# Optimization experiments

Measured on AMD Instinct MI355X. Metric: run time of the kernel, lower is better.

## Reference

```python
import jax, jax.numpy as jnp
import numpy as np

DIM = 512
INNER = 512          # heads * dim_head = 8 * 64
SCALE = 64 ** -0.5   # dim_head ** -0.5 (module uses this even though attention dim is INNER)
EPS = 1e-5


def _ln(x, g, b):
    m = jnp.mean(x, axis=-1, keepdims=True)
    v = jnp.var(x, axis=-1, keepdims=True)
    return (x - m) * jax.lax.rsqrt(v + EPS) * g + b


def setup_inputs() -> dict:
    key = jax.random.key(0)
    ks = jax.random.split(key, 5)
    B, T, C = 2, 32, 1024
    scaled = lambda k, sh, fan: jax.random.normal(k, sh, jnp.float32) * (fan ** -0.5)
    return {
        "x": jax.random.normal(ks[0], (B, T, C, DIM), jnp.float32),
        "gamma_t": jnp.ones((DIM,), jnp.float32),
        "beta_t": jnp.zeros((DIM,), jnp.float32),
        "w_qkv_t": scaled(ks[1], (DIM, 3 * INNER), DIM),
        "w_out_t": scaled(ks[2], (INNER, DIM), INNER),
        "b_out_t": jnp.zeros((DIM,), jnp.float32),
        "gamma_s": jnp.ones((DIM,), jnp.float32),
        "beta_s": jnp.zeros((DIM,), jnp.float32),
        "w_qkv_s": scaled(ks[3], (DIM, 3 * INNER), DIM),
        "w_out_s": scaled(ks[4], (INNER, DIM), INNER),
        "b_out_s": jnp.zeros((DIM,), jnp.float32),
    }


def reference(x, gamma_t, beta_t, w_qkv_t, w_out_t, b_out_t,
              gamma_s, beta_s, w_qkv_s, w_out_s, b_out_s):
    # ---- temporal attention (attend over t, per spatial token c) ----
    h = _ln(x, gamma_t, beta_t)                              # [b,t,c,D]
    q, k, v = jnp.split(h @ w_qkv_t, 3, axis=-1)             # each [b,t,c,I]
    q, k, v = (jnp.swapaxes(a, 1, 2) for a in (q, k, v))     # [b,c,t,I]
    attn = jax.nn.softmax(jnp.einsum('bcqd,bckd->bcqk', q, k) * SCALE, axis=-1)
    out = jnp.einsum('bcqk,bckd->bcqd', attn, v)             # [b,c,t,I]
    out = out @ w_out_t + b_out_t                            # [b,c,t,D]
    # ---- spatial attention (attend over c, per frame t) ----
    h = _ln(out, gamma_s, beta_s)                            # [b,c,t,D]
    q, k, v = jnp.split(h @ w_qkv_s, 3, axis=-1)             # each [b,c,t,I]
    q, k, v = (jnp.swapaxes(a, 1, 2) for a in (q, k, v))     # [b,t,c,I]
    attn = jax.nn.softmax(jnp.einsum('btqd,btkd->btqk', q, k) * SCALE, axis=-1)
    out = jnp.einsum('btqk,btkd->btqd', attn, v)             # [b,t,c,I]
    return out @ w_out_s + b_out_s                           # [b,t,c,D]
```

## Files before the change

kernel.cpp:

```cpp
#include <hip/hip_runtime.h>
#include <type_traits>

typedef unsigned short u16;
typedef _Float16 f16;
typedef f16 f16x8 __attribute__((ext_vector_type(8)));
typedef unsigned short u16x8 __attribute__((ext_vector_type(8)));
typedef unsigned short u16x4 __attribute__((ext_vector_type(4)));
typedef float f32x4 __attribute__((ext_vector_type(4)));

#define DEV __device__ __forceinline__

DEV u16 f2h(float f) { return __builtin_bit_cast(u16, (f16)f); }
DEV float h2f(u16 u) { return (float)__builtin_bit_cast(f16, u); }

DEV f32x4 mfma_f16(f16x8 a, f16x8 b, f32x4 c) {
  return __builtin_amdgcn_mfma_f32_16x16x32_f16(a, b, c, 0, 0, 0);
}
DEV f16x8 ldf16(const u16* p) { return *(const f16x8*)p; }

DEV void gl2lds16(const u16* g, u16* l) {
  __builtin_amdgcn_global_load_lds((const __attribute__((address_space(1))) void*)g,
                                   (__attribute__((address_space(3))) void*)l, 16, 0, 0);
}

DEV int swz(int row, int col) { return row * 64 + (col ^ ((row & 7) << 3)); }

DEV int xcd_remap(int d, int nwg) { return (d & 7) * (nwg >> 3) + (d >> 3); }

__global__ __launch_bounds__(256)
void wT_all_kernel(const float* __restrict__ Wq_t, const float* __restrict__ Wo_t,
                   const float* __restrict__ Wq_s, const float* __restrict__ Wo_s,
                   u16* __restrict__ Tq_t, u16* __restrict__ To_t,
                   u16* __restrict__ Tq_s, u16* __restrict__ To_s) {
  const int bid = blockIdx.x;
  const float* W;
  u16* T;
  int N, base;
  if (bid < 768)       { W = Wq_t; T = Tq_t; N = 1536; base = bid; }
  else if (bid < 1024) { W = Wo_t; T = To_t; N = 512;  base = bid - 768; }
  else if (bid < 1792) { W = Wq_s; T = Tq_s; N = 1536; base = bid - 1024; }
  else                 { W = Wo_s; T = To_s; N = 512;  base = bid - 1792; }
#pragma unroll
  for (int j = 0; j < 4; ++j) {
    int i = base * 1024 + j * 256 + threadIdx.x;
    int n = i >> 9, k = i & 511;
    T[i] = f2h(W[(size_t)k * N + n]);
  }
}

__global__ __launch_bounds__(256)
void ln_kernel(const float* __restrict__ X, const float* __restrict__ G,
               const float* __restrict__ B, u16* __restrict__ H) {
  const int row = (blockIdx.x << 2) + (threadIdx.x >> 6);
  const int l = threadIdx.x & 63;
  const float* x = X + ((size_t)row << 9) + l * 8;
  float v[8];
  *(float4*)&v[0] = *(const float4*)(x);
  *(float4*)&v[4] = *(const float4*)(x + 4);
  float s = 0.f, s2 = 0.f;
#pragma unroll
  for (int e = 0; e < 8; ++e) { s += v[e]; s2 += v[e] * v[e]; }
#pragma unroll
  for (int o = 1; o < 64; o <<= 1) { s += __shfl_xor(s, o, 64); s2 += __shfl_xor(s2, o, 64); }
  const float mean = s * (1.f / 512.f);
  const float rs = rsqrtf(s2 * (1.f / 512.f) - mean * mean + 1e-5f);
  float g[8], bb[8];
  *(float4*)&g[0] = *(const float4*)(G + l * 8);
  *(float4*)&g[4] = *(const float4*)(G + l * 8 + 4);
  *(float4*)&bb[0] = *(const float4*)(B + l * 8);
  *(float4*)&bb[4] = *(const float4*)(B + l * 8 + 4);
  u16x8 o8;
#pragma unroll
  for (int e = 0; e < 8; ++e) o8[e] = f2h((v[e] - mean) * rs * g[e] + bb[e]);
  *(u16x8*)(H + ((size_t)row << 9) + l * 8) = o8;
}

__global__ __launch_bounds__(256)
void ln16_kernel(const u16* __restrict__ X, const float* __restrict__ G,
                 const float* __restrict__ B, u16* __restrict__ H) {
  const int row = (blockIdx.x << 2) + (threadIdx.x >> 6);
  const int l = threadIdx.x & 63;
  u16x8 raw = *(const u16x8*)(X + ((size_t)row << 9) + l * 8);
  float v[8];
#pragma unroll
  for (int e = 0; e < 8; ++e) v[e] = h2f(raw[e]);
  float s = 0.f, s2 = 0.f;
#pragma unroll
  for (int e = 0; e < 8; ++e) { s += v[e]; s2 += v[e] * v[e]; }
#pragma unroll
  for (int o = 1; o < 64; o <<= 1) { s += __shfl_xor(s, o, 64); s2 += __shfl_xor(s2, o, 64); }
  const float mean = s * (1.f / 512.f);
  const float rs = rsqrtf(s2 * (1.f / 512.f) - mean * mean + 1e-5f);
  float g[8], bb[8];
  *(float4*)&g[0] = *(const float4*)(G + l * 8);
  *(float4*)&g[4] = *(const float4*)(G + l * 8 + 4);
  *(float4*)&bb[0] = *(const float4*)(B + l * 8);
  *(float4*)&bb[4] = *(const float4*)(B + l * 8 + 4);
  u16x8 o8;
#pragma unroll
  for (int e = 0; e < 8; ++e) o8[e] = f2h((v[e] - mean) * rs * g[e] + bb[e]);
  *(u16x8*)(H + ((size_t)row << 9) + l * 8) = o8;
}

template <int K>
__global__ __launch_bounds__(256)
void gemm_qkv(const u16* __restrict__ A, const u16* __restrict__ Bt,
              u16* __restrict__ Cq, u16* __restrict__ Cv, int lda, int ldb) {
  __shared__ u16 lds[2 * 128 * 64];
  u16* lsA = lds;
  u16* lsB = lds + 128 * 64;
  const int tid = threadIdx.x;
  const int w = tid >> 6, l = tid & 63;
  const int lr = l & 15, lg = l >> 4;
  const int wm = w >> 1, wn = w & 1;
  const int gx = gridDim.x;
  const int wk = xcd_remap(blockIdx.y * gx + blockIdx.x, gx * gridDim.y);
  const int Row0 = (wk / gx) * 128, Col0 = (wk % gx) * 128;
  const int gcol = ((l & 7) ^ (l >> 3)) * 8;

  const int srow = w * 32 + (l >> 3);
  const u16* baseA = A + (size_t)(Row0 + srow) * lda + gcol;
  const u16* baseB = Bt + (size_t)(Col0 + srow) * ldb + gcol;

  f32x4 acc[4][4];
  const f32x4 zero = {0.f, 0.f, 0.f, 0.f};
#pragma unroll
  for (int m = 0; m < 4; ++m)
#pragma unroll
    for (int n = 0; n < 4; ++n) acc[m][n] = zero;

#pragma unroll
  for (int k0 = 0; k0 < K; k0 += 64) {
    __syncthreads();
#pragma unroll
    for (int i = 0; i < 4; ++i) {
      gl2lds16(baseA + (size_t)(i * 8) * lda + k0, &lsA[w * 2048 + i * 512]);
      gl2lds16(baseB + (size_t)(i * 8) * ldb + k0, &lsB[w * 2048 + i * 512]);
    }
    __syncthreads();
#pragma unroll
    for (int kk = 0; kk < 64; kk += 32) {
      f16x8 af[4], bfv[4];
#pragma unroll
      for (int m = 0; m < 4; ++m)
        af[m] = ldf16(&lsA[swz(wm * 64 + m * 16 + lr, kk + 8 * lg)]);
#pragma unroll
      for (int n = 0; n < 4; ++n)
        bfv[n] = ldf16(&lsB[swz(wn * 64 + n * 16 + lr, kk + 8 * lg)]);
#pragma unroll
      for (int m = 0; m < 4; ++m)
#pragma unroll
        for (int n = 0; n < 4; ++n) acc[m][n] = mfma_f16(af[m], bfv[n], acc[m][n]);
    }
  }

  const bool isV = (Col0 >= 1024);
#pragma unroll
  for (int p = 0; p < 2; ++p) {
    __syncthreads();
    if (wm == p) {
#pragma unroll
      for (int m = 0; m < 4; ++m)
#pragma unroll
        for (int n = 0; n < 4; ++n) {
          int col = wn * 64 + n * 16 + lr;
#pragma unroll
          for (int r = 0; r < 4; ++r)
            lds[(m * 16 + lg * 4 + r) * 136 + col] = f2h(acc[m][n][r]);
        }
    }
    __syncthreads();
#pragma unroll
    for (int it = 0; it < 4; ++it) {
      int cid = it * 256 + tid;
      int rl = cid >> 4, cc = (cid & 15) * 8;
      u16x8 vv = *(u16x8*)&lds[rl * 136 + cc];
      int gr = Row0 + p * 64 + rl;
      int gc = Col0 + cc;
      if (!isV)
        *(u16x8*)&Cq[(size_t)gr * 1024 + gc] = vv;
      else
        *(u16x8*)&Cv[(size_t)gr * 512 + gc - 1024] = vv;
    }
  }
}

template <bool OUT16, bool REMAP, int K>
__global__ __launch_bounds__(256)
void gemm_bt(const u16* __restrict__ A, const u16* __restrict__ Bt,
             void* __restrict__ Cp, const float* __restrict__ bias,
             int lda, int ldb, int ldc,
             long long sA, long long sB, long long sC, float scale) {
  __shared__ u16 lds[2 * 128 * 64];
  u16* lsA = lds;
  u16* lsB = lds + 128 * 64;
  const int tid = threadIdx.x;
  const int w = tid >> 6, l = tid & 63;
  const int lr = l & 15, lg = l >> 4;
  const int wm = w >> 1, wn = w & 1;
  int Row0, Col0;
  if constexpr (REMAP) {
    const int gx = gridDim.x;
    const int wk = xcd_remap(blockIdx.y * gx + blockIdx.x, gx * gridDim.y);
    Row0 = (wk / gx) * 128; Col0 = (wk % gx) * 128;
  } else {
    Row0 = blockIdx.y * 128; Col0 = blockIdx.x * 128;
  }
  const int bz = blockIdx.z;
  const int gcol = ((l & 7) ^ (l >> 3)) * 8;

  const int srow = w * 32 + (l >> 3);
  const u16* baseA = A + (size_t)bz * sA + (size_t)(Row0 + srow) * lda + gcol;
  const u16* baseB = Bt + (size_t)bz * sB + (size_t)(Col0 + srow) * ldb + gcol;

  f32x4 acc[4][4];
  const f32x4 zero = {0.f, 0.f, 0.f, 0.f};
#pragma unroll
  for (int m = 0; m < 4; ++m)
#pragma unroll
    for (int n = 0; n < 4; ++n) acc[m][n] = zero;

#pragma unroll
  for (int k0 = 0; k0 < K; k0 += 64) {
    __syncthreads();
#pragma unroll
    for (int i = 0; i < 4; ++i) {
      gl2lds16(baseA + (size_t)(i * 8) * lda + k0, &lsA[w * 2048 + i * 512]);
      gl2lds16(baseB + (size_t)(i * 8) * ldb + k0, &lsB[w * 2048 + i * 512]);
    }
    __syncthreads();
#pragma unroll
    for (int kk = 0; kk < 64; kk += 32) {
      f16x8 af[4], bfv[4];
#pragma unroll
      for (int m = 0; m < 4; ++m)
        af[m] = ldf16(&lsA[swz(wm * 64 + m * 16 + lr, kk + 8 * lg)]);
#pragma unroll
      for (int n = 0; n < 4; ++n)
        bfv[n] = ldf16(&lsB[swz(wn * 64 + n * 16 + lr, kk + 8 * lg)]);
#pragma unroll
      for (int m = 0; m < 4; ++m)
#pragma unroll
        for (int n = 0; n < 4; ++n) acc[m][n] = mfma_f16(af[m], bfv[n], acc[m][n]);
    }
  }

  if constexpr (OUT16) {
    u16* Cb = (u16*)Cp + (size_t)bz * sC;
#pragma unroll
    for (int p = 0; p < 2; ++p) {
      __syncthreads();
      if (wm == p) {
#pragma unroll
        for (int m = 0; m < 4; ++m)
#pragma unroll
          for (int n = 0; n < 4; ++n) {
            int col = wn * 64 + n * 16 + lr;
            float bv = bias ? bias[Col0 + col] : 0.f;
#pragma unroll
            for (int r = 0; r < 4; ++r)
              lds[(m * 16 + lg * 4 + r) * 136 + col] = f2h(acc[m][n][r] * scale + bv);
          }
      }
      __syncthreads();
#pragma unroll
      for (int it = 0; it < 4; ++it) {
        int cid = it * 256 + tid;
        int rl = cid >> 4, cc = (cid & 15) * 8;
        u16x8 vv = *(u16x8*)&lds[rl * 136 + cc];
        *(u16x8*)&Cb[(size_t)(Row0 + p * 64 + rl) * ldc + Col0 + cc] = vv;
      }
    }
  } else {
    float* Cb = (float*)Cp + (size_t)bz * sC;
    float* ldsF = (float*)lds;
#pragma unroll
    for (int q = 0; q < 4; ++q) {
      __syncthreads();
      if (wm == (q >> 1)) {
        int mBase = (q & 1) * 2;
#pragma unroll
        for (int mi = 0; mi < 2; ++mi) {
          int m = mBase + mi;
#pragma unroll
          for (int n = 0; n < 4; ++n) {
            int col = wn * 64 + n * 16 + lr;
            float bv = bias ? bias[Col0 + col] : 0.f;
#pragma unroll
            for (int r = 0; r < 4; ++r)
              ldsF[(mi * 16 + lg * 4 + r) * 132 + col] = acc[m][n][r] * scale + bv;
          }
        }
      }
      __syncthreads();
#pragma unroll
      for (int it = 0; it < 4; ++it) {
        int cid = it * 256 + tid;
        int rw = cid >> 5, c4 = (cid & 31) * 4;
        float4 v = *(float4*)&ldsF[rw * 132 + c4];
        *(float4*)&Cb[(size_t)(Row0 + q * 32 + rw) * ldc + Col0 + c4] = v;
      }
    }
  }
}

__global__ __launch_bounds__(256)
void attn_t_kernel(const u16* __restrict__ QK, const u16* __restrict__ Vb,
                   u16* __restrict__ O) {
  __shared__ u16 qs[32 * 520];
  __shared__ u16 ks[32 * 520];
  __shared__ u16 vT[512 * 40];
  __shared__ float Sf[32 * 36];
  __shared__ u16 Pf[32 * 40];

  const int tid = threadIdx.x;
  const int bc = blockIdx.x;
  const int w = tid >> 6, l = tid & 63, lr = l & 15, lg = l >> 4;
  const int wr = w >> 1, wc = w & 1;
  const size_t base = (size_t)(bc >> 10) * 32768 + (bc & 1023);

#pragma unroll
  for (int i = 0; i < 8; ++i) {
    int t = w * 8 + i;
    const u16* rb = QK + (base + (size_t)t * 1024) * 1024;
    gl2lds16(rb + l * 8, &qs[t * 520]);
    gl2lds16(rb + 512 + l * 8, &ks[t * 520]);
  }
  {
    const int t = tid & 31;
    const int db0 = (tid >> 5) * 8;
    const u16* vrow = Vb + (base + (size_t)t * 1024) * 512;
#pragma unroll
    for (int j = 0; j < 8; ++j) {
      int db = db0 + j;
      u16x8 vv = *(const u16x8*)(vrow + db * 8);
#pragma unroll
      for (int e = 0; e < 8; ++e) vT[(db * 8 + e) * 40 + t] = vv[e];
    }
  }
  __syncthreads();

  f32x4 sacc = {0.f, 0.f, 0.f, 0.f};
#pragma unroll
  for (int kk = 0; kk < 512; kk += 32)
    sacc = mfma_f16(ldf16(&qs[(wr * 16 + lr) * 520 + kk + 8 * lg]),
                    ldf16(&ks[(wc * 16 + lr) * 520 + kk + 8 * lg]), sacc);
#pragma unroll
  for (int r = 0; r < 4; ++r)
    Sf[(wr * 16 + lg * 4 + r) * 36 + wc * 16 + lr] = sacc[r] * 0.125f;
  __syncthreads();

  {
    const int row = tid >> 3, c0 = (tid & 7) * 4;
    float4 sv = *(float4*)&Sf[row * 36 + c0];
    float mx = fmaxf(fmaxf(sv.x, sv.y), fmaxf(sv.z, sv.w));
#pragma unroll
    for (int o = 1; o < 8; o <<= 1) mx = fmaxf(mx, __shfl_xor(mx, o, 64));
    float e0 = __expf(sv.x - mx), e1 = __expf(sv.y - mx);
    float e2 = __expf(sv.z - mx), e3 = __expf(sv.w - mx);
    float sum = e0 + e1 + e2 + e3;
#pragma unroll
    for (int o = 1; o < 8; o <<= 1) sum += __shfl_xor(sum, o, 64);
    float inv = 1.f / sum;
    u16x4 p4 = {f2h(e0 * inv), f2h(e1 * inv), f2h(e2 * inv), f2h(e3 * inv)};
    *(u16x4*)&Pf[row * 40 + c0] = p4;
  }
  __syncthreads();

  {
    const int mr = w >> 1, nh = w & 1;
    f16x8 ap = ldf16(&Pf[(mr * 16 + lr) * 40 + 8 * lg]);
#pragma unroll
    for (int j = 0; j < 16; ++j) {
      int nc = (nh * 16 + j) * 16;
      f32x4 o = {0.f, 0.f, 0.f, 0.f};
      o = mfma_f16(ap, ldf16(&vT[(nc + lr) * 40 + 8 * lg]), o);
#pragma unroll
      for (int r = 0; r < 4; ++r)
        qs[(mr * 16 + lg * 4 + r) * 520 + nc + lr] = f2h(o[r]);
    }
  }
  __syncthreads();
#pragma unroll
  for (int it = 0; it < 8; ++it) {
    int cid = it * 256 + tid;
    int t = cid >> 6, col = (cid & 63) * 8;
    u16x8 vv = *(u16x8*)&qs[t * 520 + col];
    *(u16x8*)&O[(base + (size_t)t * 1024) * 512 + col] = vv;
  }
}

__global__ __launch_bounds__(256)
void softmax16_kernel(u16* __restrict__ S) {
  u16* p = S + ((size_t)blockIdx.x << 10);
  const int tid = threadIdx.x, w = tid >> 6, l = tid & 63;
  __shared__ float red[8];
  u16x4 raw = *(u16x4*)&p[tid << 2];
  float v0 = h2f(raw[0]), v1 = h2f(raw[1]), v2 = h2f(raw[2]), v3 = h2f(raw[3]);
  float m = fmaxf(fmaxf(v0, v1), fmaxf(v2, v3));
#pragma unroll
  for (int o = 1; o < 64; o <<= 1) m = fmaxf(m, __shfl_xor(m, o, 64));
  if (l == 0) red[w] = m;
  __syncthreads();
  m = fmaxf(fmaxf(red[0], red[1]), fmaxf(red[2], red[3]));
  v0 = __expf(v0 - m); v1 = __expf(v1 - m); v2 = __expf(v2 - m); v3 = __expf(v3 - m);
  float s = v0 + v1 + v2 + v3;
#pragma unroll
  for (int o = 1; o < 64; o <<= 1) s += __shfl_xor(s, o, 64);
  if (l == 0) red[4 + w] = s;
  __syncthreads();
  const float inv = 1.f / (red[4] + red[5] + red[6] + red[7]);
  u16x4 o4 = {f2h(v0 * inv), f2h(v1 * inv), f2h(v2 * inv), f2h(v3 * inv)};
  *(u16x4*)&p[tid << 2] = o4;
}

__global__ __launch_bounds__(256)
void transpose_v_kernel(const u16* __restrict__ Vb, u16* __restrict__ Vt) {
  __shared__ u16 tl[64][72];
  const int bt = blockIdx.z;
  const int c0 = blockIdx.x << 6, d0 = blockIdx.y << 6;
  const int tid = threadIdx.x;
#pragma unroll
  for (int pass = 0; pass < 2; ++pass) {
    int r = (pass << 5) + (tid >> 3), cc = (tid & 7) << 3;
    *(u16x8*)&tl[r][cc] = *(const u16x8*)(Vb + ((size_t)(bt * 1024 + c0 + r)) * 512 + d0 + cc);
  }
  __syncthreads();
#pragma unroll
  for (int pass = 0; pass < 2; ++pass) {
    int rd = (pass << 5) + (tid >> 3), cc = (tid & 7) << 3;
    u16x8 o;
#pragma unroll
    for (int e = 0; e < 8; ++e) o[e] = tl[cc + e][rd];
    *(u16x8*)(Vt + ((size_t)(bt * 512 + d0 + rd)) * 1024 + c0 + cc) = o;
  }
}

extern "C" void kernel_launch(void* const* d_in, const int* in_sizes, int n_in,
                              void* d_out, int out_size, void* d_ws, size_t ws_size,
                              hipStream_t stream) {
  (void)in_sizes; (void)n_in; (void)out_size; (void)ws_size;
  const float* x      = (const float*)d_in[0];
  const float* gam_t  = (const float*)d_in[1];
  const float* bet_t  = (const float*)d_in[2];
  const float* wqkv_t = (const float*)d_in[3];
  const float* wout_t = (const float*)d_in[4];
  const float* bout_t = (const float*)d_in[5];
  const float* gam_s  = (const float*)d_in[6];
  const float* bet_s  = (const float*)d_in[7];
  const float* wqkv_s = (const float*)d_in[8];
  const float* wout_s = (const float*)d_in[9];
  const float* bout_s = (const float*)d_in[10];
  float* out = (float*)d_out;

  char* ws = (char*)d_ws;
  size_t off = 0;
  auto alloc = [&](size_t bytes) -> char* {
    char* p = ws + off;
    off = (off + bytes + 255) & ~(size_t)255;
    return p;
  };
  u16* wqkvT_t = (u16*)alloc((size_t)1536 * 512 * 2);
  u16* woutT_t = (u16*)alloc((size_t)512 * 512 * 2);
  u16* wqkvT_s = (u16*)alloc((size_t)1536 * 512 * 2);
  u16* woutT_s = (u16*)alloc((size_t)512 * 512 * 2);
  u16* QK      = (u16*)alloc((size_t)65536 * 1024 * 2);
  u16* Vb      = (u16*)alloc((size_t)65536 * 512 * 2);
  u16* attnO   = (u16*)alloc((size_t)65536 * 512 * 2);
  u16* S       = (u16*)alloc((size_t)32 * 1024 * 1024 * 2);
  u16* vT      = (u16*)alloc((size_t)32 * 512 * 1024 * 2);
  u16* h       = S;
  u16* out1    = QK;

  const dim3 blk(256);

  wT_all_kernel<<<2048, blk, 0, stream>>>(wqkv_t, wout_t, wqkv_s, wout_s,
                                          wqkvT_t, woutT_t, wqkvT_s, woutT_s);

  ln_kernel<<<16384, blk, 0, stream>>>(x, gam_t, bet_t, h);
  gemm_qkv<512><<<dim3(12, 512, 1), blk, 0, stream>>>(h, wqkvT_t, QK, Vb, 512, 512);
  attn_t_kernel<<<2048, blk, 0, stream>>>(QK, Vb, attnO);
  gemm_bt<true, true, 512><<<dim3(4, 512, 1), blk, 0, stream>>>(
      attnO, woutT_t, out1, bout_t, 512, 512, 512, 0, 0, 0, 1.f);

  ln16_kernel<<<16384, blk, 0, stream>>>(out1, gam_s, bet_s, h);
  gemm_qkv<512><<<dim3(12, 512, 1), blk, 0, stream>>>(h, wqkvT_s, QK, Vb, 512, 512);

  for (int ch = 0; ch < 2; ++ch) {
    const u16* qkc = QK + (size_t)ch * 32 * 1024 * 1024;
    const u16* vbc = Vb + (size_t)ch * 32 * 1024 * 512;
    u16* attc = attnO + (size_t)ch * 32 * 1024 * 512;
    transpose_v_kernel<<<dim3(16, 8, 32), blk, 0, stream>>>(vbc, vT);
    gemm_bt<true, false, 512><<<dim3(8, 8, 32), blk, 0, stream>>>(
        qkc, qkc + 512, S, nullptr, 1024, 1024, 1024,
        1024LL * 1024, 1024LL * 1024, 1024LL * 1024, 0.125f);
    softmax16_kernel<<<32768, blk, 0, stream>>>(S);
    gemm_bt<true, false, 1024><<<dim3(4, 8, 32), blk, 0, stream>>>(
        S, vT, attc, nullptr, 1024, 1024, 512,
        1024LL * 1024, 512LL * 1024, 1024LL * 512, 1.f);
  }

  gemm_bt<false, true, 512><<<dim3(4, 512, 1), blk, 0, stream>>>(
      attnO, woutT_s, out, bout_s, 512, 512, 512, 0, 0, 0, 1.f);
}
```

Measured before the change: 862.5 us.

## Fuse V transpose into spatial QKV GEMM epilogue and XCD-remap batched GEMMs

The spatial QKV GEMM now writes its V tiles already transposed (per frame, d-major over c) through an LDS-staged epilogue. This removes the separate transpose_v kernel and its vT buffer. The batched attention GEMMs also gain a 3D XCD-aware block remapping so tiles of the same batch share L2. The cost is a transposed LDS write pattern that may have bank conflicts, and a different block order for the batched GEMMs.

After: 829.4 us. 1.04x faster.

```diff
diff --git a/kernel.cpp b/kernel.cpp
--- a/kernel.cpp
+++ b/kernel.cpp
@@ -102,7 +102,7 @@
   *(u16x8*)(H + ((size_t)row << 9) + l * 8) = o8;
 }
 
-template <int K>
+template <bool VT, int K>
 __global__ __launch_bounds__(256)
 void gemm_qkv(const u16* __restrict__ A, const u16* __restrict__ Bt,
               u16* __restrict__ Cq, u16* __restrict__ Cv, int lda, int ldb) {
@@ -155,6 +155,35 @@
   }
 
   const bool isV = (Col0 >= 1024);
+  if (VT && isV) {
+    const int bt = Row0 >> 10;
+    const int c0 = Row0 & 1023;
+    const int d0 = Col0 - 1024;
+#pragma unroll
+    for (int p = 0; p < 2; ++p) {
+      __syncthreads();
+      if (wm == p) {
+#pragma unroll
+        for (int m = 0; m < 4; ++m)
+#pragma unroll
+          for (int n = 0; n < 4; ++n) {
+            int col = wn * 64 + n * 16 + lr;
+#pragma unroll
+            for (int r = 0; r < 4; ++r)
+              lds[col * 72 + m * 16 + lg * 4 + r] = f2h(acc[m][n][r]);
+          }
+      }
+      __syncthreads();
+#pragma unroll
+      for (int it = 0; it < 4; ++it) {
+        int cid = it * 256 + tid;
+        int dl = cid >> 3, cc = (cid & 7) * 8;
+        u16x8 vv = *(u16x8*)&lds[dl * 72 + cc];
+        *(u16x8*)&Cv[(size_t)bt * 524288 + (size_t)(d0 + dl) * 1024 + c0 + p * 64 + cc] = vv;
+      }
+    }
+    return;
+  }
 #pragma unroll
   for (int p = 0; p < 2; ++p) {
     __syncthreads();
@@ -185,7 +214,7 @@
   }
 }
 
-template <bool OUT16, bool REMAP, int K>
+template <bool OUT16, int REMAP, int K>
 __global__ __launch_bounds__(256)
 void gemm_bt(const u16* __restrict__ A, const u16* __restrict__ Bt,
              void* __restrict__ Cp, const float* __restrict__ bias,
@@ -198,15 +227,22 @@
   const int w = tid >> 6, l = tid & 63;
   const int lr = l & 15, lg = l >> 4;
   const int wm = w >> 1, wn = w & 1;
-  int Row0, Col0;
-  if constexpr (REMAP) {
+  int Row0, Col0, bz;
+  if constexpr (REMAP == 1) {
     const int gx = gridDim.x;
     const int wk = xcd_remap(blockIdx.y * gx + blockIdx.x, gx * gridDim.y);
-    Row0 = (wk / gx) * 128; Col0 = (wk % gx) * 128;
+    Row0 = (wk / gx) * 128; Col0 = (wk % gx) * 128; bz = blockIdx.z;
+  } else if constexpr (REMAP == 2) {
+    const int gx = gridDim.x, gy = gridDim.y;
+    const int d = blockIdx.x + gx * (blockIdx.y + gy * blockIdx.z);
+    const int wk = xcd_remap(d, gx * gy * gridDim.z);
+    Col0 = (wk % gx) * 128;
+    int rest = wk / gx;
+    Row0 = (rest % gy) * 128;
+    bz = rest / gy;
   } else {
-    Row0 = blockIdx.y * 128; Col0 = blockIdx.x * 128;
-  }
-  const int bz = blockIdx.z;
+    Row0 = blockIdx.y * 128; Col0 = blockIdx.x * 128; bz = blockIdx.z;
+  }
   const int gcol = ((l & 7) ^ (l >> 3)) * 8;
 
   const int srow = w * 32 + (l >> 3);
@@ -412,28 +448,6 @@
   const float inv = 1.f / (red[4] + red[5] + red[6] + red[7]);
   u16x4 o4 = {f2h(v0 * inv), f2h(v1 * inv), f2h(v2 * inv), f2h(v3 * inv)};
   *(u16x4*)&p[tid << 2] = o4;
-}
-
-__global__ __launch_bounds__(256)
-void transpose_v_kernel(const u16* __restrict__ Vb, u16* __restrict__ Vt) {
-  __shared__ u16 tl[64][72];
-  const int bt = blockIdx.z;
-  const int c0 = blockIdx.x << 6, d0 = blockIdx.y << 6;
-  const int tid = threadIdx.x;
-#pragma unroll
-  for (int pass = 0; pass < 2; ++pass) {
-    int r = (pass << 5) + (tid >> 3), cc = (tid & 7) << 3;
-    *(u16x8*)&tl[r][cc] = *(const u16x8*)(Vb + ((size_t)(bt * 1024 + c0 + r)) * 512 + d0 + cc);
-  }
-  __syncthreads();
-#pragma unroll
-  for (int pass = 0; pass < 2; ++pass) {
-    int rd = (pass << 5) + (tid >> 3), cc = (tid & 7) << 3;
-    u16x8 o;
-#pragma unroll
-    for (int e = 0; e < 8; ++e) o[e] = tl[cc + e][rd];
-    *(u16x8*)(Vt + ((size_t)(bt * 512 + d0 + rd)) * 1024 + c0 + cc) = o;
-  }
 }
 
 extern "C" void kernel_launch(void* const* d_in, const int* in_sizes, int n_in,
@@ -468,9 +482,9 @@
   u16* Vb      = (u16*)alloc((size_t)65536 * 512 * 2);
   u16* attnO   = (u16*)alloc((size_t)65536 * 512 * 2);
   u16* S       = (u16*)alloc((size_t)32 * 1024 * 1024 * 2);
-  u16* vT      = (u16*)alloc((size_t)32 * 512 * 1024 * 2);
   u16* h       = S;
   u16* out1    = QK;
+  u16* Vt      = Vb;
 
   const dim3 blk(256);
 
@@ -478,28 +492,27 @@
                                           wqkvT_t, woutT_t, wqkvT_s, woutT_s);
 
   ln_kernel<<<16384, blk, 0, stream>>>(x, gam_t, bet_t, h);
-  gemm_qkv<512><<<dim3(12, 512, 1), blk, 0, stream>>>(h, wqkvT_t, QK, Vb, 512, 512);
+  gemm_qkv<false, 512><<<dim3(12, 512, 1), blk, 0, stream>>>(h, wqkvT_t, QK, Vb, 512, 512);
   attn_t_kernel<<<2048, blk, 0, stream>>>(QK, Vb, attnO);
-  gemm_bt<true, true, 512><<<dim3(4, 512, 1), blk, 0, stream>>>(
+  gemm_bt<true, 1, 512><<<dim3(4, 512, 1), blk, 0, stream>>>(
       attnO, woutT_t, out1, bout_t, 512, 512, 512, 0, 0, 0, 1.f);
 
   ln16_kernel<<<16384, blk, 0, stream>>>(out1, gam_s, bet_s, h);
-  gemm_qkv<512><<<dim3(12, 512, 1), blk, 0, stream>>>(h, wqkvT_s, QK, Vb, 512, 512);
+  gemm_qkv<true, 512><<<dim3(12, 512, 1), blk, 0, stream>>>(h, wqkvT_s, QK, Vt, 512, 512);
 
   for (int ch = 0; ch < 2; ++ch) {
     const u16* qkc = QK + (size_t)ch * 32 * 1024 * 1024;
-    const u16* vbc = Vb + (size_t)ch * 32 * 1024 * 512;
+    const u16* vtc = Vt + (size_t)ch * 32 * 512 * 1024;
     u16* attc = attnO + (size_t)ch * 32 * 1024 * 512;
-    transpose_v_kernel<<<dim3(16, 8, 32), blk, 0, stream>>>(vbc, vT);
-    gemm_bt<true, false, 512><<<dim3(8, 8, 32), blk, 0, stream>>>(
+    gemm_bt<true, 2, 512><<<dim3(8, 8, 32), blk, 0, stream>>>(
         qkc, qkc + 512, S, nullptr, 1024, 1024, 1024,
         1024LL * 1024, 1024LL * 1024, 1024LL * 1024, 0.125f);
     softmax16_kernel<<<32768, blk, 0, stream>>>(S);
-    gemm_bt<true, false, 1024><<<dim3(4, 8, 32), blk, 0, stream>>>(
-        S, vT, attc, nullptr, 1024, 1024, 512,
+    gemm_bt<true, 2, 1024><<<dim3(4, 8, 32), blk, 0, stream>>>(
+        S, vtc, attc, nullptr, 1024, 1024, 512,
         1024LL * 1024, 512LL * 1024, 1024LL * 512, 1.f);
   }
 
-  gemm_bt<false, true, 512><<<dim3(4, 512, 1), blk, 0, stream>>>(
+  gemm_bt<false, 1, 512><<<dim3(4, 512, 1), blk, 0, stream>>>(
       attnO, woutT_s, out, bout_s, 512, 512, 512, 0, 0, 0, 1.f);
 }
```
